# Kernel optimization log

Measured on AMD Instinct MI355X. Metric: run time of the kernel, lower is better.

The kernel has to match this reference:

```python
import jax, jax.numpy as jnp
import numpy as np

B, T, H, K = 256, 512, 1024, 128  # batch, seq_len, input_size, num_tags


def setup_inputs() -> dict:
    key = jax.random.key(0)
    k1, k2, k3, k4, k5, k6 = jax.random.split(key, 6)
    hiddens = jax.random.normal(k1, (B, T, H), jnp.float32)
    mask = jnp.ones((B, T), dtype=bool)  # torchcrf requires mask[:,0] all on
    labels = jax.random.randint(k2, (B, T), 0, K)
    W = jax.random.normal(k3, (K, H), jnp.float32) * 0.02  # Linear weight
    b = jnp.zeros((K,), jnp.float32)                        # Linear bias
    start_trans = jax.random.normal(k4, (K,), jnp.float32) * 0.1
    end_trans = jax.random.normal(k5, (K,), jnp.float32) * 0.1
    transitions = jax.random.normal(k6, (K, K), jnp.float32) * 0.1
    return dict(hiddens=hiddens, mask=mask, labels=labels, W=W, b=b,
                start_trans=start_trans, end_trans=end_trans,
                transitions=transitions)


def _crf_nll_mean(logits, labels, mask, start, end, trans):
    # -mean(log p(labels | logits)), matching torchcrf reduction='mean'
    maskf = mask.astype(logits.dtype)
    # numerator: score of the gold path
    emit = jnp.take_along_axis(logits, labels[..., None], axis=-1)[..., 0]  # [B,T]
    num = start[labels[:, 0]] + (emit * maskf).sum(1)
    num = num + (trans[labels[:, :-1], labels[:, 1:]] * maskf[:, 1:]).sum(1)
    last_idx = mask.sum(1).astype(jnp.int32) - 1                            # [B]
    last_tag = jnp.take_along_axis(labels, last_idx[:, None], axis=1)[:, 0]
    num = num + end[last_tag]
    # denominator: log partition via forward recurrence (log-sum-exp DP)
    em_t = jnp.swapaxes(logits, 0, 1)   # [T,B,K]
    mk_t = jnp.swapaxes(mask, 0, 1)     # [T,B]
    def step(score, xs):
        e, m = xs  # e: [B,K], m: [B]
        nxt = jax.nn.logsumexp(score[:, :, None] + trans[None] + e[:, None, :], axis=1)
        return jnp.where(m[:, None], nxt, score), None
    init = start[None, :] + em_t[0]
    score, _ = jax.lax.scan(step, init, (em_t[1:], mk_t[1:]))
    den = jax.nn.logsumexp(score + end[None, :], axis=1)
    return -(num - den).mean()


def _viterbi(logits, mask, start, end, trans):
    # max-plus forward pass with backpointers, then backtrack
    em_t = jnp.swapaxes(logits, 0, 1)   # [T,B,K]
    mk_t = jnp.swapaxes(mask, 0, 1)     # [T,B]
    K_ = trans.shape[0]
    def step(score, xs):
        e, m = xs
        bscore = score[:, :, None] + trans[None]      # [B,K,K]
        idx = jnp.argmax(bscore, axis=1)              # [B,K] backpointers
        nxt = jnp.max(bscore, axis=1) + e
        nxt = jnp.where(m[:, None], nxt, score)
        idx = jnp.where(m[:, None], idx, jnp.arange(K_)[None, :])  # pass-through when masked
        return nxt, idx
    init = start[None, :] + em_t[0]
    score, hist = jax.lax.scan(step, init, (em_t[1:], mk_t[1:]))  # hist: [T-1,B,K]
    last = jnp.argmax(score + end[None, :], axis=1)               # [B]
    def back(tag, h):
        prev = jnp.take_along_axis(h, tag[:, None], axis=1)[:, 0]
        return prev, tag  # ys[t] = tag at time t+1
    first, rest = jax.lax.scan(back, last, hist, reverse=True)
    return jnp.concatenate([first[:, None], jnp.swapaxes(rest, 0, 1)], axis=1)  # [B,T]


def reference(hiddens, mask, labels, W, b, start_trans, end_trans, transitions):
    logits = jnp.einsum('bth,kh->btk', hiddens, W) + b  # output_layer
    pred = _viterbi(logits, mask, start_trans, end_trans, transitions)
    loss = _crf_nll_mean(logits, labels, mask, start_trans, end_trans, transitions)
    return pred, loss
```

## Files before the change

### kernel.cpp

```cpp
#include <hip/hip_runtime.h>
#include <hip/hip_bf16.h>

#define Bn 256
#define Tn 512
#define Hn 1024
#define Kn 128

__device__ __forceinline__ void block_sync_lds() {
  asm volatile("s_waitcnt lgkmcnt(0)" ::: "memory");
  __builtin_amdgcn_s_barrier();
  asm volatile("" ::: "memory");
}

__device__ __forceinline__ float dpp_max8(float x) {
  int y;
  y = __builtin_amdgcn_update_dpp(__float_as_int(x), __float_as_int(x), 0xB1, 0xF, 0xF, false);
  x = fmaxf(x, __int_as_float(y));
  y = __builtin_amdgcn_update_dpp(__float_as_int(x), __float_as_int(x), 0x4E, 0xF, 0xF, false);
  x = fmaxf(x, __int_as_float(y));
  y = __builtin_amdgcn_update_dpp(__float_as_int(x), __float_as_int(x), 0x141, 0xF, 0xF, false);
  x = fmaxf(x, __int_as_float(y));
  return x;
}
__device__ __forceinline__ float dpp_add8(float x) {
  int y;
  y = __builtin_amdgcn_update_dpp(__float_as_int(x), __float_as_int(x), 0xB1, 0xF, 0xF, false);
  x = x + __int_as_float(y);
  y = __builtin_amdgcn_update_dpp(__float_as_int(x), __float_as_int(x), 0x4E, 0xF, 0xF, false);
  x = x + __int_as_float(y);
  y = __builtin_amdgcn_update_dpp(__float_as_int(x), __float_as_int(x), 0x141, 0xF, 0xF, false);
  x = x + __int_as_float(y);
  return x;
}

#define BK 32
#define LDT 132

__global__ __launch_bounds__(256) void gemm_logits(
    const float* __restrict__ A, const float* __restrict__ W,
    const float* __restrict__ bias, float* __restrict__ C)
{
  __shared__ float As[BK][LDT];
  __shared__ float Ws[BK][LDT];
  const int tid  = threadIdx.x;
  const int wv   = tid >> 6;
  const int lane = tid & 63;
  const int trow = ((wv >> 1) << 6) + (((lane >> 3) & 7) << 3);
  const int tcol = ((wv & 1) << 6) + ((lane & 7) << 3);
  const long row0 = (long)blockIdx.x * 128;

  float acc[8][8];
#pragma unroll
  for (int i = 0; i < 8; ++i)
#pragma unroll
    for (int j = 0; j < 8; ++j) acc[i][j] = 0.f;

  const int lr = tid >> 3;
  const int lk = (tid & 7) << 2;

  for (int kt = 0; kt < Hn; kt += BK) {
#pragma unroll
    for (int p = 0; p < 4; ++p) {
      const int r = lr + (p << 5);
      const float4 av = *reinterpret_cast<const float4*>(&A[(row0 + r) * Hn + kt + lk]);
      As[lk + 0][r] = av.x; As[lk + 1][r] = av.y; As[lk + 2][r] = av.z; As[lk + 3][r] = av.w;
      const float4 wv4 = *reinterpret_cast<const float4*>(&W[(long)r * Hn + kt + lk]);
      Ws[lk + 0][r] = wv4.x; Ws[lk + 1][r] = wv4.y; Ws[lk + 2][r] = wv4.z; Ws[lk + 3][r] = wv4.w;
    }
    __syncthreads();
#pragma unroll
    for (int kk = 0; kk < BK; ++kk) {
      float a[8], bv[8];
      *reinterpret_cast<float4*>(&a[0])  = *reinterpret_cast<const float4*>(&As[kk][trow]);
      *reinterpret_cast<float4*>(&a[4])  = *reinterpret_cast<const float4*>(&As[kk][trow + 4]);
      *reinterpret_cast<float4*>(&bv[0]) = *reinterpret_cast<const float4*>(&Ws[kk][tcol]);
      *reinterpret_cast<float4*>(&bv[4]) = *reinterpret_cast<const float4*>(&Ws[kk][tcol + 4]);
#pragma unroll
      for (int i = 0; i < 8; ++i)
#pragma unroll
        for (int j = 0; j < 8; ++j)
          acc[i][j] = fmaf(a[i], bv[j], acc[i][j]);
    }
    __syncthreads();
  }

  float bs[8];
#pragma unroll
  for (int j = 0; j < 8; ++j) bs[j] = bias[tcol + j];
#pragma unroll
  for (int i = 0; i < 8; ++i) {
    float4 o0, o1;
    o0.x = acc[i][0] + bs[0]; o0.y = acc[i][1] + bs[1];
    o0.z = acc[i][2] + bs[2]; o0.w = acc[i][3] + bs[3];
    o1.x = acc[i][4] + bs[4]; o1.y = acc[i][5] + bs[5];
    o1.z = acc[i][6] + bs[6]; o1.w = acc[i][7] + bs[7];
    float* cp = &C[(row0 + trow + i) * Kn + tcol];
    *reinterpret_cast<float4*>(cp)     = o0;
    *reinterpret_cast<float4*>(cp + 4) = o1;
  }
}

__global__ __launch_bounds__(256, 2) void crf_fused(
    const float* __restrict__ logits, const float* __restrict__ trans,
    const float* __restrict__ start,  const float* __restrict__ endt,
    float* __restrict__ sglob,
    int*   __restrict__ lastTag,
    float* __restrict__ den,
    const int* __restrict__ labels,
    float* __restrict__ num)
{
  const int tid  = threadIdx.x;
  const int q    = tid >> 3;
  const int g    = tid & 7;
  const int lane = tid & 63;
  const int wv   = tid >> 6;

  __shared__ __align__(16) float buf[2][Kn];
  __shared__ float mbuf[2];
  __shared__ float redv[4];
  __shared__ int   redi[4];

  if (blockIdx.x < Bn) {
    const int b = blockIdx.x;
    const float* lb = logits + (long)b * Tn * Kn;
    float Tf[16][4];
#pragma unroll
    for (int j = 0; j < 16; ++j) {
      const float4 t4 = *reinterpret_cast<const float4*>(&trans[(16 * g + j) * Kn + 4 * q]);
      Tf[j][0] = t4.x; Tf[j][1] = t4.y; Tf[j][2] = t4.z; Tf[j][3] = t4.w;
    }
    float* sg = sglob + (long)b * (Tn - 1) * Kn;
    if (tid < Kn) buf[0][tid] = start[tid] + lb[tid];
    float4 e0 = *reinterpret_cast<const float4*>(&lb[1 * Kn + 4 * q]);
    float4 e1 = *reinterpret_cast<const float4*>(&lb[2 * Kn + 4 * q]);
    float4 e2 = *reinterpret_cast<const float4*>(&lb[3 * Kn + 4 * q]);
    float4 e3 = *reinterpret_cast<const float4*>(&lb[4 * Kn + 4 * q]);
    block_sync_lds();

#define VSTEP(T, EREG, RD, WR) { \
    const float4 ev = EREG; \
    { const int tpf = ((T) + 4 <= 511) ? (T) + 4 : 511; \
      EREG = *reinterpret_cast<const float4*>(&lb[tpf * Kn + 4 * q]); } \
    float cf[16]; \
    { const float4* sp = reinterpret_cast<const float4*>(&buf[RD][g << 4]); \
      const float4 c0 = sp[0], c1 = sp[1], c2 = sp[2], c3 = sp[3]; \
      cf[0]=c0.x; cf[1]=c0.y; cf[2]=c0.z; cf[3]=c0.w; \
      cf[4]=c1.x; cf[5]=c1.y; cf[6]=c1.z; cf[7]=c1.w; \
      cf[8]=c2.x; cf[9]=c2.y; cf[10]=c2.z; cf[11]=c2.w; \
      cf[12]=c3.x; cf[13]=c3.y; cf[14]=c3.z; cf[15]=c3.w; } \
    float mx[4]; \
    _Pragma("unroll") \
    for (int s = 0; s < 4; ++s) { \
      float v[16]; \
      _Pragma("unroll") \
      for (int j = 0; j < 16; ++j) v[j] = cf[j] + Tf[j][s]; \
      _Pragma("unroll") \
      for (int w = 8; w >= 1; w >>= 1) \
        _Pragma("unroll") \
        for (int k = 0; k < w; ++k) v[k] = fmaxf(v[k], v[k + w]); \
      mx[s] = dpp_max8(v[0]); \
    } \
    if (g == 0) { \
      float4 bst; bst.x = mx[0]; bst.y = mx[1]; bst.z = mx[2]; bst.w = mx[3]; \
      *reinterpret_cast<float4*>(&sg[(long)((T) - 1) * Kn + 4 * q]) = bst; \
      float4 ns; ns.x = mx[0] + ev.x; ns.y = mx[1] + ev.y; \
      ns.z = mx[2] + ev.z; ns.w = mx[3] + ev.w; \
      *reinterpret_cast<float4*>(&buf[WR][4 * q]) = ns; \
    } \
    block_sync_lds(); \
  }

    for (int t = 1; t <= 505; t += 4) {
      VSTEP(t + 0, e0, 0, 1)
      VSTEP(t + 1, e1, 1, 0)
      VSTEP(t + 2, e2, 0, 1)
      VSTEP(t + 3, e3, 1, 0)
    }
    VSTEP(509, e0, 0, 1)
    VSTEP(510, e1, 1, 0)
    VSTEP(511, e2, 0, 1)
#undef VSTEP

    float lv2 = -__FLT_MAX__; int la = 0;
    if (tid < Kn) { lv2 = buf[1][tid] + endt[tid]; la = tid; }
#pragma unroll
    for (int o = 32; o > 0; o >>= 1) {
      const float xv = __shfl_xor(lv2, o);
      const int   xa = __shfl_xor(la, o);
      if (xv > lv2 || (xv == lv2 && xa < la)) { lv2 = xv; la = xa; }
    }
    if (lane == 0) { redv[wv] = lv2; redi[wv] = la; }
    __syncthreads();
    if (tid == 0) {
      float bvv = redv[0]; int bai = redi[0];
#pragma unroll
      for (int w = 1; w < 4; ++w)
        if (redv[w] > bvv || (redv[w] == bvv && redi[w] < bai)) { bvv = redv[w]; bai = redi[w]; }
      lastTag[b] = bai;
    }
  } else if (blockIdx.x < 2 * Bn) {
    const int b = blockIdx.x - Bn;
    const float* lb = logits + (long)b * Tn * Kn;
    float Mf[16][4];
#pragma unroll
    for (int j = 0; j < 16; ++j) {
      const float4 t4 = *reinterpret_cast<const float4*>(&trans[(16 * g + j) * Kn + 4 * q]);
      Mf[j][0] = __expf(t4.x); Mf[j][1] = __expf(t4.y);
      Mf[j][2] = __expf(t4.z); Mf[j][3] = __expf(t4.w);
    }
    float s0, s1, s2, s3;
    {
      const float4 st4 = *reinterpret_cast<const float4*>(&start[4 * q]);
      const float4 l4  = *reinterpret_cast<const float4*>(&lb[4 * q]);
      s0 = st4.x + l4.x; s1 = st4.y + l4.y; s2 = st4.z + l4.z; s3 = st4.w + l4.w;
    }
    if (tid == 0) mbuf[1] = s0;
    float4 e0 = *reinterpret_cast<const float4*>(&lb[1 * Kn + 4 * q]);
    float4 e1 = *reinterpret_cast<const float4*>(&lb[2 * Kn + 4 * q]);
    float4 e2 = *reinterpret_cast<const float4*>(&lb[3 * Kn + 4 * q]);
    float4 e3 = *reinterpret_cast<const float4*>(&lb[4 * Kn + 4 * q]);
    block_sync_lds();

#define FSTEP(T, EREG, PB) { \
    const float m = mbuf[PB]; \
    if (g == 0) { \
      float4 p; p.x = __expf(s0 - m); p.y = __expf(s1 - m); \
      p.z = __expf(s2 - m); p.w = __expf(s3 - m); \
      *reinterpret_cast<float4*>(&buf[PB][4 * q]) = p; \
    } \
    if (tid == 0) mbuf[PB ^ 1] = s0; \
    const float4 ev = EREG; \
    { const int tpf = ((T) + 4 <= 511) ? (T) + 4 : 511; \
      EREG = *reinterpret_cast<const float4*>(&lb[tpf * Kn + 4 * q]); } \
    block_sync_lds(); \
    float cf[16]; \
    { const float4* sp = reinterpret_cast<const float4*>(&buf[PB][g << 4]); \
      const float4 c0 = sp[0], c1 = sp[1], c2 = sp[2], c3 = sp[3]; \
      cf[0]=c0.x; cf[1]=c0.y; cf[2]=c0.z; cf[3]=c0.w; \
      cf[4]=c1.x; cf[5]=c1.y; cf[6]=c1.z; cf[7]=c1.w; \
      cf[8]=c2.x; cf[9]=c2.y; cf[10]=c2.z; cf[11]=c2.w; \
      cf[12]=c3.x; cf[13]=c3.y; cf[14]=c3.z; cf[15]=c3.w; } \
    float ac0 = 0.f, ac1 = 0.f, ac2 = 0.f, ac3 = 0.f; \
    _Pragma("unroll") \
    for (int j = 0; j < 16; ++j) { \
      ac0 = fmaf(cf[j], Mf[j][0], ac0); ac1 = fmaf(cf[j], Mf[j][1], ac1); \
      ac2 = fmaf(cf[j], Mf[j][2], ac2); ac3 = fmaf(cf[j], Mf[j][3], ac3); \
    } \
    ac0 = dpp_add8(ac0); ac1 = dpp_add8(ac1); \
    ac2 = dpp_add8(ac2); ac3 = dpp_add8(ac3); \
    s0 = m + __logf(ac0) + ev.x; s1 = m + __logf(ac1) + ev.y; \
    s2 = m + __logf(ac2) + ev.z; s3 = m + __logf(ac3) + ev.w; \
  }

    for (int t = 1; t <= 505; t += 4) {
      FSTEP(t + 0, e0, 1)
      FSTEP(t + 1, e1, 0)
      FSTEP(t + 2, e2, 1)
      FSTEP(t + 3, e3, 0)
    }
    FSTEP(509, e0, 1)
    FSTEP(510, e1, 0)
    FSTEP(511, e2, 1)
#undef FSTEP

    if (g == 0) {
      float4 sv4; sv4.x = s0; sv4.y = s1; sv4.z = s2; sv4.w = s3;
      *reinterpret_cast<float4*>(&buf[0][4 * q]) = sv4;
    }
    __syncthreads();
    float v = -__FLT_MAX__;
    if (tid < Kn) v = buf[0][tid] + endt[tid];
    float m2 = v;
#pragma unroll
    for (int o = 32; o > 0; o >>= 1) m2 = fmaxf(m2, __shfl_xor(m2, o));
    if (lane == 0) redv[wv] = m2;
    __syncthreads();
    m2 = fmaxf(fmaxf(redv[0], redv[1]), fmaxf(redv[2], redv[3]));
    float pv = (tid < Kn) ? __expf(v - m2) : 0.f;
#pragma unroll
    for (int o = 32; o > 0; o >>= 1) pv += __shfl_xor(pv, o);
    __syncthreads();
    if (lane == 0) redv[wv] = pv;
    __syncthreads();
    if (tid == 0) den[b] = m2 + __logf(redv[0] + redv[1] + redv[2] + redv[3]);
  } else {
    const int b = blockIdx.x - 2 * Bn;
    const int* lab = labels + (long)b * Tn;
    const float* lbn = logits + (long)b * Tn * Kn;
    float acc = 0.f;
    for (int t = tid; t < Tn; t += 256) {
      const int l = lab[t];
      acc += lbn[(long)t * Kn + l];
      if (t + 1 < Tn) acc += trans[l * Kn + lab[t + 1]];
    }
#pragma unroll
    for (int o = 32; o > 0; o >>= 1) acc += __shfl_xor(acc, o);
    if (lane == 0) redv[wv] = acc;
    __syncthreads();
    if (tid == 0)
      num[b] = redv[0] + redv[1] + redv[2] + redv[3] + start[lab[0]] + endt[lab[Tn - 1]];
  }
}

__global__ __launch_bounds__(64) void crf_backtrack(
    const float* __restrict__ trans, const float* __restrict__ sglob,
    const float* __restrict__ logits, const float* __restrict__ start,
    const int* __restrict__ lastTag, float* __restrict__ pred)
{
  __shared__ float tl[Kn][132];
  const int b = blockIdx.x, lane = threadIdx.x;
  for (int idx = lane; idx < Kn * Kn; idx += 64) {
    const int k = idx >> 7, kp = idx & 127;
    tl[kp][k] = trans[idx];
  }
  block_sync_lds();

  const float* sg = sglob + (long)b * (Tn - 1) * Kn;
  const float* lg = logits + (long)b * Tn * Kn;
  float* po = pred + (long)b * Tn;

  int tag = lastTag[b];
  if (lane == 0) po[Tn - 1] = (float)tag;
  float target;
  {
    const float tb0 = sg[510 * Kn + lane], tb1 = sg[510 * Kn + 64 + lane];
    const float r0 = __int_as_float(__builtin_amdgcn_readlane(__float_as_int(tb0), tag & 63));
    const float r1 = __int_as_float(__builtin_amdgcn_readlane(__float_as_int(tb1), tag & 63));
    target = (tag < 64) ? r0 : r1;
  }

#define LOADROW(T, B0, B1, E0, E1) { \
    const int t_ = (T); \
    E0 = lg[t_ * Kn + lane]; E1 = lg[t_ * Kn + 64 + lane]; \
    B0 = (t_ > 0) ? sg[(t_ - 1) * Kn + lane]      : start[lane]; \
    B1 = (t_ > 0) ? sg[(t_ - 1) * Kn + 64 + lane] : start[64 + lane]; \
  }
#define BSTEP(T, B0, B1, E0, E1) { \
    const float* trow = &tl[tag][0]; \
    const float c0 = (B0 + E0) + trow[lane]; \
    const float c1 = (B1 + E1) + trow[64 + lane]; \
    const unsigned long long m0 = __ballot(c0 == target); \
    const unsigned long long m1 = __ballot(c1 == target); \
    const int nt = m0 ? (__ffsll((unsigned long long)m0) - 1) \
                      : (64 + __ffsll((unsigned long long)m1) - 1); \
    const float r0 = __int_as_float(__builtin_amdgcn_readlane(__float_as_int(B0), nt & 63)); \
    const float r1 = __int_as_float(__builtin_amdgcn_readlane(__float_as_int(B1), nt & 63)); \
    target = (nt < 64) ? r0 : r1; \
    tag = nt; \
    if (lane == 0) po[T] = (float)tag; \
    { const int tp = (T) - 4; if (tp >= 0) LOADROW(tp, B0, B1, E0, E1) } \
  }

  float b00, b01, e00, e01;
  float b10, b11, e10, e11;
  float b20, b21, e20, e21;
  float b30, b31, e30, e31;
  LOADROW(510, b00, b01, e00, e01)
  LOADROW(509, b10, b11, e10, e11)
  LOADROW(508, b20, b21, e20, e21)
  LOADROW(507, b30, b31, e30, e31)

  for (int t = 510; t >= 6; t -= 4) {
    BSTEP(t - 0, b00, b01, e00, e01)
    BSTEP(t - 1, b10, b11, e10, e11)
    BSTEP(t - 2, b20, b21, e20, e21)
    BSTEP(t - 3, b30, b31, e30, e31)
  }
  BSTEP(2, b00, b01, e00, e01)
  BSTEP(1, b10, b11, e10, e11)
  BSTEP(0, b20, b21, e20, e21)
#undef BSTEP
#undef LOADROW
}

__global__ __launch_bounds__(256) void loss_kernel(
    const float* __restrict__ den, const float* __restrict__ num,
    float* __restrict__ out)
{
  const int tid = threadIdx.x;
  const int wv = tid >> 6, lane = tid & 63;
  __shared__ float r4[4];
  float v = den[tid] - num[tid];
#pragma unroll
  for (int o = 32; o > 0; o >>= 1) v += __shfl_xor(v, o);
  if (lane == 0) r4[wv] = v;
  __syncthreads();
  if (tid == 0) out[Bn * Tn] = (r4[0] + r4[1] + r4[2] + r4[3]) * (1.0f / Bn);
}

extern "C" void kernel_launch(void* const* d_in, const int* in_sizes, int n_in,
                              void* d_out, int out_size, void* d_ws, size_t ws_size,
                              hipStream_t stream) {
  const float* hiddens = (const float*)d_in[0];
  const int*   labels  = (const int*)d_in[2];
  const float* W       = (const float*)d_in[3];
  const float* bias    = (const float*)d_in[4];
  const float* start   = (const float*)d_in[5];
  const float* endt    = (const float*)d_in[6];
  const float* trans   = (const float*)d_in[7];
  float* out = (float*)d_out;

  char* ws = (char*)d_ws;
  float* logits  = (float*)ws;
  float* sglob   = (float*)(ws + (size_t)67108864);
  int*   lastT   = (int*)  (ws + (size_t)67108864 + 66977792);
  float* den     = (float*)(ws + (size_t)67108864 + 66977792 + 1024);
  float* num     = den + Bn;

  gemm_logits  <<<dim3((Bn * Tn) / 128), dim3(256), 0, stream>>>(hiddens, W, bias, logits);
  crf_fused    <<<dim3(3 * Bn), dim3(256), 0, stream>>>(logits, trans, start, endt, sglob,
                                                        lastT, den, labels, num);
  crf_backtrack<<<dim3(Bn), dim3(64), 0, stream>>>(trans, sglob, logits, start, lastT, out);
  loss_kernel  <<<dim3(1),  dim3(256), 0, stream>>>(den, num, out);
}
```

Before: 842.0 us.

## Fuse Viterbi backtrack and gold-path numerator into the CRF forward kernel

The separate backtrack kernel is removed. Its work now runs in wave 0 of each Viterbi block right after the forward pass, reading a transposed transition table built in shared memory. The gold-path numerator moves into the tail of the partition-function blocks, so the launch shrinks from 3B to 2B blocks and one kernel launch plus the lastTag round trip disappear. The log-sum-exp inner product also splits into two accumulator chains to shorten FMA dependency latency. In exchange, each block allocates about 68KB of extra LDS, which may lower occupancy, and the backtrack runs on one wave while three waves idle.

```diff
diff --git a/kernel.cpp b/kernel.cpp
--- a/kernel.cpp
+++ b/kernel.cpp
@@ -104,10 +104,10 @@
     const float* __restrict__ logits, const float* __restrict__ trans,
     const float* __restrict__ start,  const float* __restrict__ endt,
     float* __restrict__ sglob,
-    int*   __restrict__ lastTag,
     float* __restrict__ den,
     const int* __restrict__ labels,
-    float* __restrict__ num)
+    float* __restrict__ num,
+    float* __restrict__ pred)
 {
   const int tid  = threadIdx.x;
   const int q    = tid >> 3;
@@ -116,6 +116,7 @@
   const int wv   = tid >> 6;
 
   __shared__ __align__(16) float buf[2][Kn];
+  __shared__ float tl[Kn][133];
   __shared__ float mbuf[2];
   __shared__ float redv[4];
   __shared__ int   redi[4];
@@ -190,15 +191,73 @@
       if (xv > lv2 || (xv == lv2 && xa < la)) { lv2 = xv; la = xa; }
     }
     if (lane == 0) { redv[wv] = lv2; redi[wv] = la; }
-    __syncthreads();
-    if (tid == 0) {
-      float bvv = redv[0]; int bai = redi[0];
+
+    for (int idx = tid; idx < Kn * Kn; idx += 256) {
+      const int k = idx >> 7, kp = idx & 127;
+      tl[kp][k] = trans[idx];
+    }
+    __syncthreads();
+
+    if (wv == 0) {
+      float bvv = redv[0]; int tag = redi[0];
 #pragma unroll
       for (int w = 1; w < 4; ++w)
-        if (redv[w] > bvv || (redv[w] == bvv && redi[w] < bai)) { bvv = redv[w]; bai = redi[w]; }
-      lastTag[b] = bai;
-    }
-  } else if (blockIdx.x < 2 * Bn) {
+        if (redv[w] > bvv || (redv[w] == bvv && redi[w] < tag)) { bvv = redv[w]; tag = redi[w]; }
+      const float* lg = lb;
+      float* po = pred + (long)b * Tn;
+      if (lane == 0) po[Tn - 1] = (float)tag;
+      float target;
+      {
+        const float tb0 = sg[510 * Kn + lane], tb1 = sg[510 * Kn + 64 + lane];
+        const float r0 = __int_as_float(__builtin_amdgcn_readlane(__float_as_int(tb0), tag & 63));
+        const float r1 = __int_as_float(__builtin_amdgcn_readlane(__float_as_int(tb1), tag & 63));
+        target = (tag < 64) ? r0 : r1;
+      }
+
+#define LOADROW(T, B0, B1, E0, E1) { \
+      const int t_ = (T); \
+      E0 = lg[t_ * Kn + lane]; E1 = lg[t_ * Kn + 64 + lane]; \
+      B0 = (t_ > 0) ? sg[(t_ - 1) * Kn + lane]      : start[lane]; \
+      B1 = (t_ > 0) ? sg[(t_ - 1) * Kn + 64 + lane] : start[64 + lane]; \
+    }
+#define BSTEP(T, B0, B1, E0, E1) { \
+      const float* trow = &tl[tag][0]; \
+      const float c0 = (B0 + E0) + trow[lane]; \
+      const float c1 = (B1 + E1) + trow[64 + lane]; \
+      const unsigned long long m0 = __ballot(c0 == target); \
+      const unsigned long long m1 = __ballot(c1 == target); \
+      const int nt = m0 ? (__ffsll((unsigned long long)m0) - 1) \
+                        : (64 + __ffsll((unsigned long long)m1) - 1); \
+      const float r0 = __int_as_float(__builtin_amdgcn_readlane(__float_as_int(B0), nt & 63)); \
+      const float r1 = __int_as_float(__builtin_amdgcn_readlane(__float_as_int(B1), nt & 63)); \
+      target = (nt < 64) ? r0 : r1; \
+      tag = nt; \
+      if (lane == 0) po[T] = (float)tag; \
+      { const int tp = (T) - 4; if (tp >= 0) LOADROW(tp, B0, B1, E0, E1) } \
+    }
+
+      float b00, b01, e00, e01;
+      float b10, b11, e10, e11;
+      float b20, b21, e20, e21;
+      float b30, b31, e30, e31;
+      LOADROW(510, b00, b01, e00, e01)
+      LOADROW(509, b10, b11, e10, e11)
+      LOADROW(508, b20, b21, e20, e21)
+      LOADROW(507, b30, b31, e30, e31)
+
+      for (int t = 510; t >= 6; t -= 4) {
+        BSTEP(t - 0, b00, b01, e00, e01)
+        BSTEP(t - 1, b10, b11, e10, e11)
+        BSTEP(t - 2, b20, b21, e20, e21)
+        BSTEP(t - 3, b30, b31, e30, e31)
+      }
+      BSTEP(2, b00, b01, e00, e01)
+      BSTEP(1, b10, b11, e10, e11)
+      BSTEP(0, b20, b21, e20, e21)
+#undef BSTEP
+#undef LOADROW
+    }
+  } else {
     const int b = blockIdx.x - Bn;
     const float* lb = logits + (long)b * Tn * Kn;
     float Mf[16][4];
@@ -240,12 +299,16 @@
       cf[4]=c1.x; cf[5]=c1.y; cf[6]=c1.z; cf[7]=c1.w; \
       cf[8]=c2.x; cf[9]=c2.y; cf[10]=c2.z; cf[11]=c2.w; \
       cf[12]=c3.x; cf[13]=c3.y; cf[14]=c3.z; cf[15]=c3.w; } \
-    float ac0 = 0.f, ac1 = 0.f, ac2 = 0.f, ac3 = 0.f; \
+    float a0A = 0.f, a1A = 0.f, a2A = 0.f, a3A = 0.f; \
+    float a0B = 0.f, a1B = 0.f, a2B = 0.f, a3B = 0.f; \
     _Pragma("unroll") \
-    for (int j = 0; j < 16; ++j) { \
-      ac0 = fmaf(cf[j], Mf[j][0], ac0); ac1 = fmaf(cf[j], Mf[j][1], ac1); \
-      ac2 = fmaf(cf[j], Mf[j][2], ac2); ac3 = fmaf(cf[j], Mf[j][3], ac3); \
+    for (int j = 0; j < 8; ++j) { \
+      a0A = fmaf(cf[j], Mf[j][0], a0A); a1A = fmaf(cf[j], Mf[j][1], a1A); \
+      a2A = fmaf(cf[j], Mf[j][2], a2A); a3A = fmaf(cf[j], Mf[j][3], a3A); \
+      a0B = fmaf(cf[8 + j], Mf[8 + j][0], a0B); a1B = fmaf(cf[8 + j], Mf[8 + j][1], a1B); \
+      a2B = fmaf(cf[8 + j], Mf[8 + j][2], a2B); a3B = fmaf(cf[8 + j], Mf[8 + j][3], a3B); \
     } \
+    float ac0 = a0A + a0B, ac1 = a1A + a1B, ac2 = a2A + a2B, ac3 = a3A + a3B; \
     ac0 = dpp_add8(ac0); ac1 = dpp_add8(ac1); \
     ac2 = dpp_add8(ac2); ac3 = dpp_add8(ac3); \
     s0 = m + __logf(ac0) + ev.x; s1 = m + __logf(ac1) + ev.y; \
@@ -283,14 +346,13 @@
     if (lane == 0) redv[wv] = pv;
     __syncthreads();
     if (tid == 0) den[b] = m2 + __logf(redv[0] + redv[1] + redv[2] + redv[3]);
-  } else {
-    const int b = blockIdx.x - 2 * Bn;
+
+    __syncthreads();
     const int* lab = labels + (long)b * Tn;
-    const float* lbn = logits + (long)b * Tn * Kn;
     float acc = 0.f;
     for (int t = tid; t < Tn; t += 256) {
       const int l = lab[t];
-      acc += lbn[(long)t * Kn + l];
+      acc += lb[(long)t * Kn + l];
       if (t + 1 < Tn) acc += trans[l * Kn + lab[t + 1]];
     }
 #pragma unroll
@@ -300,77 +362,6 @@
     if (tid == 0)
       num[b] = redv[0] + redv[1] + redv[2] + redv[3] + start[lab[0]] + endt[lab[Tn - 1]];
   }
-}
-
-__global__ __launch_bounds__(64) void crf_backtrack(
-    const float* __restrict__ trans, const float* __restrict__ sglob,
-    const float* __restrict__ logits, const float* __restrict__ start,
-    const int* __restrict__ lastTag, float* __restrict__ pred)
-{
-  __shared__ float tl[Kn][132];
-  const int b = blockIdx.x, lane = threadIdx.x;
-  for (int idx = lane; idx < Kn * Kn; idx += 64) {
-    const int k = idx >> 7, kp = idx & 127;
-    tl[kp][k] = trans[idx];
-  }
-  block_sync_lds();
-
-  const float* sg = sglob + (long)b * (Tn - 1) * Kn;
-  const float* lg = logits + (long)b * Tn * Kn;
-  float* po = pred + (long)b * Tn;
-
-  int tag = lastTag[b];
-  if (lane == 0) po[Tn - 1] = (float)tag;
-  float target;
-  {
-    const float tb0 = sg[510 * Kn + lane], tb1 = sg[510 * Kn + 64 + lane];
-    const float r0 = __int_as_float(__builtin_amdgcn_readlane(__float_as_int(tb0), tag & 63));
-    const float r1 = __int_as_float(__builtin_amdgcn_readlane(__float_as_int(tb1), tag & 63));
-    target = (tag < 64) ? r0 : r1;
-  }
-
-#define LOADROW(T, B0, B1, E0, E1) { \
-    const int t_ = (T); \
-    E0 = lg[t_ * Kn + lane]; E1 = lg[t_ * Kn + 64 + lane]; \
-    B0 = (t_ > 0) ? sg[(t_ - 1) * Kn + lane]      : start[lane]; \
-    B1 = (t_ > 0) ? sg[(t_ - 1) * Kn + 64 + lane] : start[64 + lane]; \
-  }
-#define BSTEP(T, B0, B1, E0, E1) { \
-    const float* trow = &tl[tag][0]; \
-    const float c0 = (B0 + E0) + trow[lane]; \
-    const float c1 = (B1 + E1) + trow[64 + lane]; \
-    const unsigned long long m0 = __ballot(c0 == target); \
-    const unsigned long long m1 = __ballot(c1 == target); \
-    const int nt = m0 ? (__ffsll((unsigned long long)m0) - 1) \
-                      : (64 + __ffsll((unsigned long long)m1) - 1); \
-    const float r0 = __int_as_float(__builtin_amdgcn_readlane(__float_as_int(B0), nt & 63)); \
-    const float r1 = __int_as_float(__builtin_amdgcn_readlane(__float_as_int(B1), nt & 63)); \
-    target = (nt < 64) ? r0 : r1; \
-    tag = nt; \
-    if (lane == 0) po[T] = (float)tag; \
-    { const int tp = (T) - 4; if (tp >= 0) LOADROW(tp, B0, B1, E0, E1) } \
-  }
-
-  float b00, b01, e00, e01;
-  float b10, b11, e10, e11;
-  float b20, b21, e20, e21;
-  float b30, b31, e30, e31;
-  LOADROW(510, b00, b01, e00, e01)
-  LOADROW(509, b10, b11, e10, e11)
-  LOADROW(508, b20, b21, e20, e21)
-  LOADROW(507, b30, b31, e30, e31)
-
-  for (int t = 510; t >= 6; t -= 4) {
-    BSTEP(t - 0, b00, b01, e00, e01)
-    BSTEP(t - 1, b10, b11, e10, e11)
-    BSTEP(t - 2, b20, b21, e20, e21)
-    BSTEP(t - 3, b30, b31, e30, e31)
-  }
-  BSTEP(2, b00, b01, e00, e01)
-  BSTEP(1, b10, b11, e10, e11)
-  BSTEP(0, b20, b21, e20, e21)
-#undef BSTEP
-#undef LOADROW
 }
 
 __global__ __launch_bounds__(256) void loss_kernel(
@@ -403,13 +394,11 @@
   char* ws = (char*)d_ws;
   float* logits  = (float*)ws;
   float* sglob   = (float*)(ws + (size_t)67108864);
-  int*   lastT   = (int*)  (ws + (size_t)67108864 + 66977792);
-  float* den     = (float*)(ws + (size_t)67108864 + 66977792 + 1024);
-  float* num     = den + Bn;
-
-  gemm_logits  <<<dim3((Bn * Tn) / 128), dim3(256), 0, stream>>>(hiddens, W, bias, logits);
-  crf_fused    <<<dim3(3 * Bn), dim3(256), 0, stream>>>(logits, trans, start, endt, sglob,
-                                                        lastT, den, labels, num);
-  crf_backtrack<<<dim3(Bn), dim3(64), 0, stream>>>(trans, sglob, logits, start, lastT, out);
-  loss_kernel  <<<dim3(1),  dim3(256), 0, stream>>>(den, num, out);
-}
+  float* den     = (float*)(ws + (size_t)134086656);
+  float* num     = (float*)(ws + (size_t)134087680);
+
+  gemm_logits<<<dim3((Bn * Tn) / 128), dim3(256), 0, stream>>>(hiddens, W, bias, logits);
+  crf_fused  <<<dim3(2 * Bn), dim3(256), 0, stream>>>(logits, trans, start, endt, sglob,
+                                                      den, labels, num, out);
+  loss_kernel<<<dim3(1), dim3(256), 0, stream>>>(den, num, out);
+}
```

After: 780.9 us. 7.3% less time.
